# Performance work log

Hardware: AMD Instinct MI355X
Metric: run time of the kernel (lower is better)

## Reference

```python
import jax, jax.numpy as jnp
import numpy as np

ATOM_FEAT_DIM = 32
HIDDEN = 512
N = 4096


def _linear_params(key, in_dim, out_dim):
    kw, kb = jax.random.split(key)
    bound = 1.0 / np.sqrt(in_dim)
    W = jax.random.uniform(kw, (out_dim, in_dim), minval=-bound, maxval=bound, dtype=jnp.float32)
    b = jax.random.uniform(kb, (out_dim,), minval=-bound, maxval=bound, dtype=jnp.float32)
    return W, b


def setup_inputs() -> dict:
    key = jax.random.key(0)
    ks = jax.random.split(key, 8)
    x = jax.random.normal(ks[0], (N, ATOM_FEAT_DIM), dtype=jnp.float32)
    adj = jax.random.uniform(ks[1], (N, N), dtype=jnp.float32)
    w_self1, b_self1 = _linear_params(ks[2], ATOM_FEAT_DIM, HIDDEN)
    w_neigh1, b_neigh1 = _linear_params(ks[3], ATOM_FEAT_DIM, HIDDEN)
    w_self2, b_self2 = _linear_params(ks[4], HIDDEN, HIDDEN)
    w_neigh2, b_neigh2 = _linear_params(ks[5], HIDDEN, HIDDEN)
    w_atom, b_atom = _linear_params(ks[6], HIDDEN, ATOM_FEAT_DIM)
    w_bond, b_bond = _linear_params(ks[7], 2 * HIDDEN, 4)
    return dict(x=x, adj=adj,
                w_self1=w_self1, b_self1=b_self1, w_neigh1=w_neigh1, b_neigh1=b_neigh1,
                w_self2=w_self2, b_self2=b_self2, w_neigh2=w_neigh2, b_neigh2=b_neigh2,
                w_atom=w_atom, b_atom=b_atom, w_bond=w_bond, b_bond=b_bond)


def _graph_conv(x, adj, w_self, b_self, w_neigh, b_neigh):
    deg = jnp.clip(adj.sum(axis=-1, keepdims=True), 1.0, None)  # (N,1)
    agg = (adj @ x) / deg
    return jax.nn.relu(x @ w_self.T + b_self + agg @ w_neigh.T + b_neigh)


def reference(x, adj, w_self1, b_self1, w_neigh1, b_neigh1,
              w_self2, b_self2, w_neigh2, b_neigh2,
              w_atom, b_atom, w_bond, b_bond):
    h1 = _graph_conv(x, adj, w_self1, b_self1, w_neigh1, b_neigh1)
    h2 = _graph_conv(h1, adj, w_self2, b_self2, w_neigh2, b_neigh2)  # (N,H)
    atom_logits = h2 @ w_atom.T + b_atom  # (N,F)
    # bond_head(cat(h2[i],h2[j])) = h2[i]@W[:, :H].T + h2[j]@W[:, H:].T + b
    H = h2.shape[1]
    a = h2 @ w_bond[:, :H].T  # (N,4) contribution of node i
    b = h2 @ w_bond[:, H:].T  # (N,4) contribution of node j
    upper = a[:, None, :] + b[None, :, :] + b_bond  # logits for pair (i,j)
    n = h2.shape[0]
    iu = jnp.triu(jnp.ones((n, n), dtype=h2.dtype), k=1)[:, :, None]  # i<j mask
    # original fills bond[i,j]=bond[j,i]=logits(i,j) for i<j; diagonal stays zero
    bond_logits = upper * iu + jnp.swapaxes(upper, 0, 1) * jnp.swapaxes(iu, 0, 1)
    return atom_logits, bond_logits
```

## Files before the change

kernel.cpp:

```cpp
#include <hip/hip_runtime.h>

#define N_ATOMS 4096
#define FDIM 32
#define HID 512

typedef __bf16 bf16x8 __attribute__((ext_vector_type(8)));
typedef float f32x4 __attribute__((ext_vector_type(4)));

__device__ __forceinline__ float bf2f(ushort h) {
  union { uint u; float f; } v; v.u = ((uint)h) << 16; return v.f;
}
__device__ __forceinline__ ushort f2bf(float f) {
  union { float f; uint u; } v; v.f = f;
  uint u = v.u;
  u += 0x7fffu + ((u >> 16) & 1u);
  return (ushort)(u >> 16);
}

__device__ __forceinline__ void gload16(const ushort* g, ushort* l) {
  __builtin_amdgcn_global_load_lds(
      (const __attribute__((address_space(1))) void*)g,
      (__attribute__((address_space(3))) void*)l,
      16, 0, 0);
}

__global__ __launch_bounds__(256) void prep_adj(const float* __restrict__ adj,
                                                ushort* __restrict__ adjb,
                                                float* __restrict__ rdeg) {
  const int row = blockIdx.x;
  const int t = threadIdx.x;
  const float* r = adj + (size_t)row * N_ATOMS;
  ushort* w = adjb + (size_t)row * N_ATOMS;
  float s = 0.f;
#pragma unroll
  for (int i = 0; i < 4; i++) {
    const int c = (t + i * 256) * 4;
    float4 v = *(const float4*)(r + c);
    s += v.x + v.y + v.z + v.w;
    ushort4 o;
    o.x = f2bf(v.x); o.y = f2bf(v.y); o.z = f2bf(v.z); o.w = f2bf(v.w);
    *(ushort4*)(w + c) = o;
  }
#pragma unroll
  for (int off = 32; off; off >>= 1) s += __shfl_down(s, off);
  __shared__ float red[4];
  if ((t & 63) == 0) red[t >> 6] = s;
  __syncthreads();
  if (t == 0) rdeg[row] = 1.f / fmaxf(red[0] + red[1] + red[2] + red[3], 1.f);
}

__global__ __launch_bounds__(256) void prep_x(const float* __restrict__ x,
                                              ushort* __restrict__ xt) {
  const int idx = blockIdx.x * 256 + threadIdx.x;
  const int m = idx >> 5, c = idx & 31;
  xt[(size_t)c * N_ATOMS + m] = f2bf(x[(size_t)m * FDIM + c]);
}

__global__ __launch_bounds__(256) void prep_w2(const float* __restrict__ ws2,
                                               const float* __restrict__ wn2,
                                               ushort* __restrict__ wcat2) {
  const int idx = blockIdx.x * 256 + threadIdx.x;
  const int n = idx >> 10, k = idx & 1023;
  float v = (k < 512) ? ws2[(size_t)n * 512 + k] : wn2[(size_t)n * 512 + k - 512];
  wcat2[idx] = f2bf(v);
}

template<int BM, int BN, int WROWS, int WCOLS>
__global__ __launch_bounds__(256, 2) void gemm_nt(
    const ushort* __restrict__ A, int lda,
    const ushort* __restrict__ B, int ldb,
    int Kchunk, float* __restrict__ Cout, int ldc, size_t cstride)
{
  constexpr int WTM = BM / WROWS;
  constexpr int WTN = BN / WCOLS;
  constexpr int MT = WTM / 16;
  constexpr int NT = WTN / 16;
  constexpr int AL = BM / 32;
  constexpr int BL = BN / 32;

  __shared__ __align__(16) ushort As[BM * 64];
  __shared__ __align__(16) ushort Bs[BN * 64];

  const int t = threadIdx.x;
  const int wave = t >> 6;
  const int lane = t & 63;
  const int q = lane >> 4;
  const int ln = lane & 15;
  const int wr = wave / WCOLS;
  const int wc = wave % WCOLS;
  const int mbase = wr * WTM;
  const int nbase = wc * WTN;

  const int n0 = blockIdx.x * BN;
  const int m0 = blockIdx.y * BM;
  const int kbase = blockIdx.z * Kchunk;
  float* __restrict__ Cs = Cout + (size_t)blockIdx.z * cstride;

  f32x4 acc[MT][NT];
#pragma unroll
  for (int i = 0; i < MT; i++)
#pragma unroll
    for (int j = 0; j < NT; j++)
#pragma unroll
      for (int r = 0; r < 4; r++) acc[i][j][r] = 0.f;

  for (int kt = 0; kt < Kchunk; kt += 64) {
    const int kg = kbase + kt;
#pragma unroll
    for (int i = 0; i < AL; i++) {
      const int g = (wave * AL + i) * 64 + lane;
      const int row = g >> 3, c8 = g & 7;
      gload16(A + (size_t)(m0 + row) * lda + kg + c8 * 8, &As[g * 8]);
    }
#pragma unroll
    for (int i = 0; i < BL; i++) {
      const int g = (wave * BL + i) * 64 + lane;
      const int row = g >> 3, c8 = g & 7;
      gload16(B + (size_t)(n0 + row) * ldb + kg + c8 * 8, &Bs[g * 8]);
    }
    __syncthreads();
#pragma unroll
    for (int kk = 0; kk < 64; kk += 32) {
      bf16x8 af[MT], bfr[NT];
#pragma unroll
      for (int i = 0; i < MT; i++)
        af[i] = *(const bf16x8*)(&As[(mbase + i * 16 + ln) * 64 + kk + q * 8]);
#pragma unroll
      for (int j = 0; j < NT; j++)
        bfr[j] = *(const bf16x8*)(&Bs[(nbase + j * 16 + ln) * 64 + kk + q * 8]);
#pragma unroll
      for (int i = 0; i < MT; i++)
#pragma unroll
        for (int j = 0; j < NT; j++)
          acc[i][j] = __builtin_amdgcn_mfma_f32_16x16x32_bf16(af[i], bfr[j], acc[i][j], 0, 0, 0);
    }
    __syncthreads();
  }

#pragma unroll
  for (int i = 0; i < MT; i++)
#pragma unroll
    for (int j = 0; j < NT; j++)
#pragma unroll
      for (int r = 0; r < 4; r++) {
        const int m = m0 + mbase + i * 16 + q * 4 + r;
        const int n = n0 + nbase + j * 16 + ln;
        Cs[(size_t)m * ldc + n] = acc[i][j][r];
      }
}

__global__ __launch_bounds__(256) void red_agg1(const float* __restrict__ sl,
                                                float* __restrict__ agg1) {
  const int idx = blockIdx.x * 256 + threadIdx.x;
  f32x4 s = {0.f, 0.f, 0.f, 0.f};
#pragma unroll
  for (int z = 0; z < 16; z++) {
    f32x4 v = *(const f32x4*)(sl + (size_t)z * N_ATOMS * FDIM + (size_t)idx * 4);
    s += v;
  }
  *(f32x4*)(agg1 + (size_t)idx * 4) = s;
}

__global__ __launch_bounds__(256) void epi_agg2(const float* __restrict__ sl,
                                                const float* __restrict__ rdeg,
                                                ushort* __restrict__ cat2) {
  const int idx = blockIdx.x * 256 + threadIdx.x;
  const int m = idx >> 7;
  const int n4 = (idx & 127) * 4;
  f32x4 s = {0.f, 0.f, 0.f, 0.f};
#pragma unroll
  for (int z = 0; z < 4; z++) {
    f32x4 v = *(const f32x4*)(sl + (size_t)z * N_ATOMS * HID + (size_t)m * HID + n4);
    s += v;
  }
  const float r = rdeg[m];
  ushort4 o;
  o.x = f2bf(s[0] * r); o.y = f2bf(s[1] * r);
  o.z = f2bf(s[2] * r); o.w = f2bf(s[3] * r);
  *(ushort4*)(cat2 + (size_t)m * 1024 + 512 + n4) = o;
}

__global__ __launch_bounds__(256) void epi_h2(const float* __restrict__ sl,
                                              const float* __restrict__ bs2,
                                              const float* __restrict__ bn2,
                                              float* __restrict__ h2f) {
  const int idx = blockIdx.x * 256 + threadIdx.x;
  const int m = idx >> 7;
  const int n4 = (idx & 127) * 4;
  f32x4 s = {0.f, 0.f, 0.f, 0.f};
#pragma unroll
  for (int z = 0; z < 4; z++) {
    f32x4 v = *(const f32x4*)(sl + (size_t)z * N_ATOMS * HID + (size_t)m * HID + n4);
    s += v;
  }
  float4 b0 = *(const float4*)(bs2 + n4);
  float4 b1 = *(const float4*)(bn2 + n4);
  f32x4 o;
  o[0] = fmaxf(s[0] + b0.x + b1.x, 0.f);
  o[1] = fmaxf(s[1] + b0.y + b1.y, 0.f);
  o[2] = fmaxf(s[2] + b0.z + b1.z, 0.f);
  o[3] = fmaxf(s[3] + b0.w + b1.w, 0.f);
  *(f32x4*)(h2f + (size_t)m * HID + n4) = o;
}

__global__ __launch_bounds__(256) void h1_kernel(
    const float* __restrict__ x, const float* __restrict__ agg1,
    const float* __restrict__ rdeg,
    const float* __restrict__ ws1, const float* __restrict__ bs1,
    const float* __restrict__ wn1, const float* __restrict__ bn1,
    ushort* __restrict__ cat2, ushort* __restrict__ h1t)
{
  const int idx = blockIdx.x * 256 + threadIdx.x;
  const int m = idx >> 9;
  const int n = idx & 511;
  const float* xr = x + (size_t)m * FDIM;
  const float* ar = agg1 + (size_t)m * FDIM;
  const float* w1 = ws1 + (size_t)n * FDIM;
  const float* w2 = wn1 + (size_t)n * FDIM;
  float accs = 0.f, accn = 0.f;
#pragma unroll
  for (int k = 0; k < FDIM; k += 4) {
    float4 xv = *(const float4*)(xr + k);
    float4 av = *(const float4*)(ar + k);
    float4 wv = *(const float4*)(w1 + k);
    float4 nv = *(const float4*)(w2 + k);
    accs += xv.x * wv.x + xv.y * wv.y + xv.z * wv.z + xv.w * wv.w;
    accn += av.x * nv.x + av.y * nv.y + av.z * nv.z + av.w * nv.w;
  }
  float v = fmaxf(accs + accn * rdeg[m] + bs1[n] + bn1[n], 0.f);
  ushort h = f2bf(v);
  cat2[(size_t)m * 1024 + n] = h;
  h1t[(size_t)n * N_ATOMS + m] = h;
}

__global__ __launch_bounds__(256) void heads_kernel(
    const float* __restrict__ h2f,
    const float* __restrict__ w_atom, const float* __restrict__ b_atom,
    const float* __restrict__ w_bond, const float* __restrict__ b_bond,
    float* __restrict__ atom_out,
    float* __restrict__ a_buf, float* __restrict__ b_buf)
{
  const int idx = blockIdx.x * 256 + threadIdx.x;
  if (idx >= N_ATOMS * 40) return;
  const int m = idx / 40;
  const int c = idx - m * 40;
  const float* hr = h2f + (size_t)m * HID;
  const float* wr;
  if (c < 32)      wr = w_atom + (size_t)c * HID;
  else if (c < 36) wr = w_bond + (size_t)(c - 32) * 1024;
  else             wr = w_bond + (size_t)(c - 36) * 1024 + 512;
  float acc = 0.f;
#pragma unroll 4
  for (int k = 0; k < HID; k += 4) {
    float4 hv = *(const float4*)(hr + k);
    float4 w0 = *(const float4*)(wr + k);
    acc += hv.x * w0.x + hv.y * w0.y + hv.z * w0.z + hv.w * w0.w;
  }
  if (c < 32)      atom_out[(size_t)m * 32 + c] = acc + b_atom[c];
  else if (c < 36) a_buf[(size_t)m * 4 + (c - 32)] = acc + b_bond[c - 32];
  else             b_buf[(size_t)m * 4 + (c - 36)] = acc;
}

__global__ __launch_bounds__(256) void bond_fill(
    const float* __restrict__ av, const float* __restrict__ bv,
    float* __restrict__ out)
{
  const int idx = blockIdx.x * 256 + threadIdx.x;
  const int i = idx >> 12;
  const int j = idx & 4095;
  float4 r;
  if (i < j) {
    float4 ai = *(const float4*)(av + (size_t)i * 4);
    float4 bj = *(const float4*)(bv + (size_t)j * 4);
    r.x = ai.x + bj.x; r.y = ai.y + bj.y;
    r.z = ai.z + bj.z; r.w = ai.w + bj.w;
  } else if (i > j) {
    float4 aj = *(const float4*)(av + (size_t)j * 4);
    float4 bi = *(const float4*)(bv + (size_t)i * 4);
    r.x = aj.x + bi.x; r.y = aj.y + bi.y;
    r.z = aj.z + bi.z; r.w = aj.w + bi.w;
  } else {
    r.x = r.y = r.z = r.w = 0.f;
  }
  *(float4*)(out + (size_t)idx * 4) = r;
}

extern "C" void kernel_launch(void* const* d_in, const int* in_sizes, int n_in,
                              void* d_out, int out_size, void* d_ws, size_t ws_size,
                              hipStream_t stream)
{
  const float* x        = (const float*)d_in[0];
  const float* adj      = (const float*)d_in[1];
  const float* w_self1  = (const float*)d_in[2];
  const float* b_self1  = (const float*)d_in[3];
  const float* w_neigh1 = (const float*)d_in[4];
  const float* b_neigh1 = (const float*)d_in[5];
  const float* w_self2  = (const float*)d_in[6];
  const float* b_self2  = (const float*)d_in[7];
  const float* w_neigh2 = (const float*)d_in[8];
  const float* b_neigh2 = (const float*)d_in[9];
  const float* w_atom   = (const float*)d_in[10];
  const float* b_atom   = (const float*)d_in[11];
  const float* w_bond   = (const float*)d_in[12];
  const float* b_bond   = (const float*)d_in[13];

  char* w = (char*)d_ws;
  float*  rdeg  = (float*)w;  w += (size_t)N_ATOMS * sizeof(float);
  float*  agg1  = (float*)w;  w += (size_t)N_ATOMS * FDIM * sizeof(float);
  float*  a_buf = (float*)w;  w += (size_t)N_ATOMS * 4 * sizeof(float);
  float*  b_buf = (float*)w;  w += (size_t)N_ATOMS * 4 * sizeof(float);
  ushort* adjb  = (ushort*)w; w += (size_t)N_ATOMS * N_ATOMS * sizeof(ushort);
  ushort* xt    = (ushort*)w; w += (size_t)FDIM * N_ATOMS * sizeof(ushort);
  ushort* h1t   = (ushort*)w; w += (size_t)HID * N_ATOMS * sizeof(ushort);
  ushort* cat2  = (ushort*)w; w += (size_t)N_ATOMS * 1024 * sizeof(ushort);
  ushort* wcat2 = (ushort*)w; w += (size_t)HID * 1024 * sizeof(ushort);
  float*  h2f   = (float*)w;  w += (size_t)N_ATOMS * HID * sizeof(float);
  float*  sl    = (float*)w;  w += (size_t)4 * N_ATOMS * HID * sizeof(float);

  float* atom_out = (float*)d_out;
  float* bond_out = (float*)d_out + (size_t)N_ATOMS * FDIM;

  prep_adj<<<N_ATOMS, 256, 0, stream>>>(adj, adjb, rdeg);
  prep_x<<<(N_ATOMS * FDIM) / 256, 256, 0, stream>>>(x, xt);
  prep_w2<<<(HID * 1024) / 256, 256, 0, stream>>>(w_self2, w_neigh2, wcat2);

  gemm_nt<128, 32, 4, 1><<<dim3(1, 32, 16), 256, 0, stream>>>(
      adjb, N_ATOMS, xt, N_ATOMS, 256, sl, FDIM, (size_t)N_ATOMS * FDIM);
  red_agg1<<<(N_ATOMS * FDIM / 4) / 256, 256, 0, stream>>>(sl, agg1);
  h1_kernel<<<(N_ATOMS * HID) / 256, 256, 0, stream>>>(
      x, agg1, rdeg, w_self1, b_self1, w_neigh1, b_neigh1, cat2, h1t);
  gemm_nt<128, 128, 2, 2><<<dim3(4, 32, 4), 256, 0, stream>>>(
      adjb, N_ATOMS, h1t, N_ATOMS, 1024, sl, HID, (size_t)N_ATOMS * HID);
  epi_agg2<<<(N_ATOMS * HID / 4) / 256, 256, 0, stream>>>(sl, rdeg, cat2);
  gemm_nt<128, 128, 2, 2><<<dim3(4, 32, 4), 256, 0, stream>>>(
      cat2, 1024, wcat2, 1024, 256, sl, HID, (size_t)N_ATOMS * HID);
  epi_h2<<<(N_ATOMS * HID / 4) / 256, 256, 0, stream>>>(sl, b_self2, b_neigh2, h2f);
  heads_kernel<<<(N_ATOMS * 40 + 255) / 256, 256, 0, stream>>>(
      h2f, w_atom, b_atom, w_bond, b_bond, atom_out, a_buf, b_buf);
  bond_fill<<<(N_ATOMS * N_ATOMS) / 256, 256, 0, stream>>>(a_buf, b_buf, bond_out);
}
```

Before: 557.6 us.

## Swizzle GEMM workgroup order, retile third GEMM, merge prep kernels

GEMM launches become 1D grids whose block index is remapped across the 8 XCDs, so neighbouring tiles sharing A/B data land on the same chiplet's L2. The third GEMM switches to 128x64 tiles with split-K of 2 instead of 4, which halves the partial-sum traffic its epilogue has to reduce. The two small preprocessing kernels are fused into one launch. The swizzle assumes the workgroup count divides evenly by 8, and the smaller tiles lower per-block reuse.

```diff
diff --git a/kernel.cpp b/kernel.cpp
--- a/kernel.cpp
+++ b/kernel.cpp
@@ -49,23 +49,24 @@
   if (t == 0) rdeg[row] = 1.f / fmaxf(red[0] + red[1] + red[2] + red[3], 1.f);
 }
 
-__global__ __launch_bounds__(256) void prep_x(const float* __restrict__ x,
-                                              ushort* __restrict__ xt) {
-  const int idx = blockIdx.x * 256 + threadIdx.x;
-  const int m = idx >> 5, c = idx & 31;
-  xt[(size_t)c * N_ATOMS + m] = f2bf(x[(size_t)m * FDIM + c]);
-}
-
-__global__ __launch_bounds__(256) void prep_w2(const float* __restrict__ ws2,
-                                               const float* __restrict__ wn2,
-                                               ushort* __restrict__ wcat2) {
-  const int idx = blockIdx.x * 256 + threadIdx.x;
-  const int n = idx >> 10, k = idx & 1023;
-  float v = (k < 512) ? ws2[(size_t)n * 512 + k] : wn2[(size_t)n * 512 + k - 512];
-  wcat2[idx] = f2bf(v);
-}
-
-template<int BM, int BN, int WROWS, int WCOLS>
+__global__ __launch_bounds__(256) void prep_misc(const float* __restrict__ x,
+                                                 ushort* __restrict__ xt,
+                                                 const float* __restrict__ ws2,
+                                                 const float* __restrict__ wn2,
+                                                 ushort* __restrict__ wcat2) {
+  const int idx = blockIdx.x * 256 + threadIdx.x;
+  if (idx < N_ATOMS * FDIM) {
+    const int m = idx >> 5, c = idx & 31;
+    xt[(size_t)c * N_ATOMS + m] = f2bf(x[(size_t)m * FDIM + c]);
+  } else {
+    const int j = idx - N_ATOMS * FDIM;
+    const int n = j >> 10, k = j & 1023;
+    float v = (k < 512) ? ws2[(size_t)n * 512 + k] : wn2[(size_t)n * 512 + k - 512];
+    wcat2[j] = f2bf(v);
+  }
+}
+
+template<int BM, int BN, int WROWS, int WCOLS, int GX, int GZ>
 __global__ __launch_bounds__(256, 2) void gemm_nt(
     const ushort* __restrict__ A, int lda,
     const ushort* __restrict__ B, int ldb,
@@ -77,9 +78,16 @@
   constexpr int NT = WTN / 16;
   constexpr int AL = BM / 32;
   constexpr int BL = BN / 32;
+  constexpr int NWG = GX * 32 * GZ;
 
   __shared__ __align__(16) ushort As[BM * 64];
   __shared__ __align__(16) ushort Bs[BN * 64];
+
+  const int id = blockIdx.x;
+  const int swz = (id & 7) * (NWG / 8) + (id >> 3);
+  const int bx = swz % GX;
+  const int by = (swz / GX) % 32;
+  const int bz = swz / (GX * 32);
 
   const int t = threadIdx.x;
   const int wave = t >> 6;
@@ -91,10 +99,10 @@
   const int mbase = wr * WTM;
   const int nbase = wc * WTN;
 
-  const int n0 = blockIdx.x * BN;
-  const int m0 = blockIdx.y * BM;
-  const int kbase = blockIdx.z * Kchunk;
-  float* __restrict__ Cs = Cout + (size_t)blockIdx.z * cstride;
+  const int n0 = bx * BN;
+  const int m0 = by * BM;
+  const int kbase = bz * Kchunk;
+  float* __restrict__ Cs = Cout + (size_t)bz * cstride;
 
   f32x4 acc[MT][NT];
 #pragma unroll
@@ -189,7 +197,7 @@
   const int n4 = (idx & 127) * 4;
   f32x4 s = {0.f, 0.f, 0.f, 0.f};
 #pragma unroll
-  for (int z = 0; z < 4; z++) {
+  for (int z = 0; z < 2; z++) {
     f32x4 v = *(const f32x4*)(sl + (size_t)z * N_ATOMS * HID + (size_t)m * HID + n4);
     s += v;
   }
@@ -321,19 +329,19 @@
   float* bond_out = (float*)d_out + (size_t)N_ATOMS * FDIM;
 
   prep_adj<<<N_ATOMS, 256, 0, stream>>>(adj, adjb, rdeg);
-  prep_x<<<(N_ATOMS * FDIM) / 256, 256, 0, stream>>>(x, xt);
-  prep_w2<<<(HID * 1024) / 256, 256, 0, stream>>>(w_self2, w_neigh2, wcat2);
-
-  gemm_nt<128, 32, 4, 1><<<dim3(1, 32, 16), 256, 0, stream>>>(
+  prep_misc<<<(N_ATOMS * FDIM + HID * 1024) / 256, 256, 0, stream>>>(
+      x, xt, w_self2, w_neigh2, wcat2);
+
+  gemm_nt<128, 32, 4, 1, 1, 16><<<512, 256, 0, stream>>>(
       adjb, N_ATOMS, xt, N_ATOMS, 256, sl, FDIM, (size_t)N_ATOMS * FDIM);
   red_agg1<<<(N_ATOMS * FDIM / 4) / 256, 256, 0, stream>>>(sl, agg1);
   h1_kernel<<<(N_ATOMS * HID) / 256, 256, 0, stream>>>(
       x, agg1, rdeg, w_self1, b_self1, w_neigh1, b_neigh1, cat2, h1t);
-  gemm_nt<128, 128, 2, 2><<<dim3(4, 32, 4), 256, 0, stream>>>(
+  gemm_nt<128, 128, 2, 2, 4, 4><<<512, 256, 0, stream>>>(
       adjb, N_ATOMS, h1t, N_ATOMS, 1024, sl, HID, (size_t)N_ATOMS * HID);
   epi_agg2<<<(N_ATOMS * HID / 4) / 256, 256, 0, stream>>>(sl, rdeg, cat2);
-  gemm_nt<128, 128, 2, 2><<<dim3(4, 32, 4), 256, 0, stream>>>(
-      cat2, 1024, wcat2, 1024, 256, sl, HID, (size_t)N_ATOMS * HID);
+  gemm_nt<128, 64, 2, 2, 8, 2><<<512, 256, 0, stream>>>(
+      cat2, 1024, wcat2, 1024, 512, sl, HID, (size_t)N_ATOMS * HID);
   epi_h2<<<(N_ATOMS * HID / 4) / 256, 256, 0, stream>>>(sl, b_self2, b_neigh2, h2f);
   heads_kernel<<<(N_ATOMS * 40 + 255) / 256, 256, 0, stream>>>(
       h2f, w_atom, b_atom, w_bond, b_bond, atom_out, a_buf, b_buf);
```

After: 552.5 us. No clear change (-0.9%).
